# Optimization experiments

Measured on AMD Instinct MI355X. Metric: run time of the kernel, lower is better.

The kernel has to match this reference:

```python
import jax, jax.numpy as jnp
from jax import lax
import numpy as np

NEG = -1e30  # safe log-space -inf for fp32 (avoids inf-inf NaNs)
EPS = 1e-7   # keras.backend.epsilon()


def setup_inputs() -> dict:
    key = jax.random.key(0)
    k1, k2 = jax.random.split(key)
    B, T, C, L = 512, 512, 96, 64
    y_true = jax.random.randint(k1, (B, L), 0, C - 1, dtype=jnp.int64)  # labels in [0, C-2]
    # y_pred mimics softmax output: positive, rows sum to 1
    logits = jax.random.uniform(k2, (B, T, C), dtype=jnp.float32)
    y_pred = logits / jnp.sum(logits, axis=-1, keepdims=True)
    return {"y_true": y_true, "y_pred": y_pred}


def _ctc_batch_cost(y_true, y_pred):
    # Faithful to keras.backend.ctc_batch_cost with full input/label lengths
    # and blank index = num_classes - 1.
    B, T, C = y_pred.shape
    L = y_true.shape[1]
    blank = C - 1
    S = 2 * L + 1  # extended label length: blanks interleaved

    logp = jnp.log(y_pred + EPS)  # [B, T, C]

    # extended label sequence: blank, l0, blank, l1, ..., blank
    ext = jnp.full((B, S), blank, dtype=y_true.dtype).at[:, 1::2].set(y_true)  # [B, S]

    # log-probs of extended labels at every time step: [T, B, S]
    lp = jnp.take_along_axis(
        logp, jnp.broadcast_to(ext[:, None, :], (B, T, S)), axis=2
    ).transpose(1, 0, 2)

    # skip transition (s-2 -> s) allowed iff ext[s] != blank and ext[s] != ext[s-2]
    skip = jnp.concatenate(
        [jnp.zeros((B, 2), dtype=bool),
         (ext[:, 2:] != blank) & (ext[:, 2:] != ext[:, :-2])],
        axis=1,
    )  # [B, S]

    # init: alpha_0(0) = logp(blank), alpha_0(1) = logp(l0)
    alpha0 = jnp.full((B, S), NEG, dtype=logp.dtype)
    alpha0 = alpha0.at[:, 0].set(lp[0, :, 0]).at[:, 1].set(lp[0, :, 1])

    def step(alpha, lp_t):
        s1 = jnp.pad(alpha[:, :-1], ((0, 0), (1, 0)), constant_values=NEG)
        s2 = jnp.pad(alpha[:, :-2], ((0, 0), (2, 0)), constant_values=NEG)
        a = jnp.logaddexp(alpha, s1)
        a = jnp.where(skip, jnp.logaddexp(a, s2), a)
        return a + lp_t, None

    alpha, _ = lax.scan(step, alpha0, lp[1:])
    loss = -jnp.logaddexp(alpha[:, -1], alpha[:, -2])  # [B]
    return loss[:, None]  # [B, 1], matching ctc_batch_cost


def reference(y_true, y_pred):
    return _ctc_batch_cost(y_true, y_pred)
```

## Files before the change

### kernel.cpp

```cpp
#include <hip/hip_runtime.h>
#include <math.h>


constexpr int Bv = 512;
constexpr int Tv = 512;
constexpr int Cv = 96;
constexpr int Lv = 64;
constexpr int BLANK = Cv - 1;
constexpr float EPSf = 1e-7f;

constexpr int ROWS = 32;
constexpr int NCH  = Tv / ROWS;
constexpr int CF   = ROWS * Cv;

__device__ __forceinline__ float dpp_shr1(float x) {
    return __int_as_float(
        __builtin_amdgcn_update_dpp(0, __float_as_int(x), 0x138, 0xf, 0xf, true));
}
template <int C>
__device__ __forceinline__ float dppmax(float m) {
    return fmaxf(m, __int_as_float(
        __builtin_amdgcn_update_dpp(0, __float_as_int(m), C, 0xf, 0xf, true)));
}

__global__ void __launch_bounds__(64) ctc_fwd(const int* __restrict__ y_true,
                                              const float* __restrict__ y_pred,
                                              float* __restrict__ out) {
    __shared__ float sink_lds[CF];

    const int b = blockIdx.x;
    const int l = threadIdx.x;
    const float* __restrict__ yp = y_pred + (size_t)b * (Tv * Cv);

    const int lab   = y_true[b * Lv + l];
    const int labm1 = __shfl_up(lab, 1);
    const bool skip = (l > 0) && (lab != labm1);

    const float* __restrict__ gB = yp + BLANK;
    const float* __restrict__ gL = yp + lab;

    float4 G0,G1,G2,G3,G4,G5,G6,G7,G8,G9,G10,G11;
    float4 H0,H1,H2,H3,H4,H5,H6,H7,H8,H9,H10,H11;
#define GLOAD(S, g) do { const float* gp_ = (g) + l * 4;                     \
    S##0 = *(const float4*)(gp_ +    0); S##1 = *(const float4*)(gp_ +  256);\
    S##2 = *(const float4*)(gp_ +  512); S##3 = *(const float4*)(gp_ +  768);\
    S##4 = *(const float4*)(gp_ + 1024); S##5 = *(const float4*)(gp_ + 1280);\
    S##6 = *(const float4*)(gp_ + 1536); S##7 = *(const float4*)(gp_ + 1792);\
    S##8 = *(const float4*)(gp_ + 2048); S##9 = *(const float4*)(gp_ + 2304);\
    S##10= *(const float4*)(gp_ + 2560); S##11= *(const float4*)(gp_ + 2816);\
    } while (0)
#define SINK(S) do { float4* sp_ = (float4*)sink_lds + l;                    \
    sp_[0]   = S##0; sp_[64]  = S##1; sp_[128] = S##2; sp_[192] = S##3;      \
    sp_[256] = S##4; sp_[320] = S##5; sp_[384] = S##6; sp_[448] = S##7;      \
    sp_[512] = S##8; sp_[576] = S##9; sp_[640] = S##10; sp_[704] = S##11;    \
    } while (0)

    GLOAD(G, yp);
    GLOAD(H, yp + CF);

    float PB0,PB1,PB2,PB3,PB4,PB5,PB6,PB7, PL0,PL1,PL2,PL3,PL4,PL5,PL6,PL7;
    float QB0,QB1,QB2,QB3,QB4,QB5,QB6,QB7, QL0,QL1,QL2,QL3,QL4,QL5,QL6,QL7;
#define LOADG(P, g) do {                                                     \
    const float* pB_ = gB + (size_t)(8 * (g)) * Cv;                          \
    const float* pL_ = gL + (size_t)(8 * (g)) * Cv;                          \
    P##B0 = pB_[0*Cv]; P##L0 = pL_[0*Cv]; P##B1 = pB_[1*Cv]; P##L1 = pL_[1*Cv];\
    P##B2 = pB_[2*Cv]; P##L2 = pL_[2*Cv]; P##B3 = pB_[3*Cv]; P##L3 = pL_[3*Cv];\
    P##B4 = pB_[4*Cv]; P##L4 = pL_[4*Cv]; P##B5 = pB_[5*Cv]; P##L5 = pL_[5*Cv];\
    P##B6 = pB_[6*Cv]; P##L6 = pL_[6*Cv]; P##B7 = pB_[7*Cv]; P##L7 = pL_[7*Cv];\
    } while (0)

    LOADG(P, 0);
    LOADG(Q, 1);

    float a0, a1, a2;
    int   e_acc = 0;
    float sc_p = 1.0f; int e_p = 0;

    auto step = [&](float PB, float PL) {
        float pb  = PB + EPSf;
        float pl  = PL + EPSf;
        float a1p = dpp_shr1(a1);
        float na0 = (a0 + a1p) * pb;
        float s1  = a0 + a1 + (skip ? a1p : 0.0f);
        float na1 = s1 * pl;
        float na2 = (a2 + a1) * pb;
        a0 = na0; a1 = na1; a2 = na2;
    };
    auto rn_apply = [&]() {
        a0 *= sc_p; a1 *= sc_p; a2 *= sc_p; e_acc += e_p;
    };
    auto rn_compute = [&]() {
        float m = fmaxf(fmaxf(a0, a1), a2);
        m = dppmax<0x111>(m); m = dppmax<0x112>(m); m = dppmax<0x114>(m);
        m = dppmax<0x118>(m); m = dppmax<0x142>(m); m = dppmax<0x143>(m);
        float mw = __int_as_float(__builtin_amdgcn_readlane(__float_as_int(m), 63));
        unsigned ef = __float_as_uint(mw) >> 23;
        e_p  = (int)ef - 126;
        sc_p = __uint_as_float((253u - ef) << 23);
    };

#define STEP_PF(P, i) do { step(P##B##i, P##L##i);                           \
    P##B##i = pB2[(i) * Cv]; P##L##i = pL2[(i) * Cv]; } while (0)
#define GROUP(P, g) do {                                                     \
    int r20_ = 8 * ((g) + 2); if (r20_ > Tv - 8) r20_ = Tv - 8;              \
    const float* pB2 = gB + (size_t)r20_ * Cv;                               \
    const float* pL2 = gL + (size_t)r20_ * Cv;                               \
    STEP_PF(P,0); STEP_PF(P,1); STEP_PF(P,2); STEP_PF(P,3); rn_apply();      \
    STEP_PF(P,4); STEP_PF(P,5); STEP_PF(P,6); STEP_PF(P,7); rn_compute();    \
    } while (0)

    {
        const bool lane0 = (l == 0);
        a0 = lane0 ? (PB0 + EPSf) : 0.0f;
        a1 = lane0 ? (PL0 + EPSf) : 0.0f;
        a2 = 0.0f;
        const float* pB2 = gB + (size_t)16 * Cv;
        const float* pL2 = gL + (size_t)16 * Cv;
        PB0 = pB2[0]; PL0 = pL2[0];
        STEP_PF(P,1); STEP_PF(P,2); STEP_PF(P,3); rn_apply();
        STEP_PF(P,4); STEP_PF(P,5); STEP_PF(P,6); STEP_PF(P,7); rn_compute();
    }

    SINK(G); GLOAD(G, yp + 2 * CF);
    GROUP(Q, 1); GROUP(P, 2); GROUP(Q, 3);

    for (int c = 1; c < NCH; ++c) {
        if (c <= NCH - 3) {
            if (c & 1) { SINK(H); GLOAD(H, yp + (size_t)(c + 2) * CF); }
            else       { SINK(G); GLOAD(G, yp + (size_t)(c + 2) * CF); }
        }
        int g = 4 * c;
        GROUP(P, g); GROUP(Q, g + 1); GROUP(P, g + 2); GROUP(Q, g + 3);
    }

    if (l == 63) {
        float sum = a1 + a2;
        out[b] = -(logf(sum) + (float)e_acc * 0.69314718055994530942f);
    }
#undef GLOAD
#undef SINK
#undef LOADG
#undef STEP_PF
#undef GROUP
}

extern "C" void kernel_launch(void* const* d_in, const int* in_sizes, int n_in,
                              void* d_out, int out_size, void* d_ws, size_t ws_size,
                              hipStream_t stream) {
    const int*   y_true = (const int*)d_in[0];
    const float* y_pred = (const float*)d_in[1];
    float*       out    = (float*)d_out;
    (void)in_sizes; (void)n_in; (void)out_size; (void)d_ws; (void)ws_size;
    ctc_fwd<<<Bv, 64, 0, stream>>>(y_true, y_pred, out);
}
```

Measured before the change: 158.8 us.

## Split into producer waves streaming y_pred chunks into an LDS ring for a consumer wave

```diff
diff --git a/kernel.cpp b/kernel.cpp
--- a/kernel.cpp
+++ b/kernel.cpp
@@ -12,6 +12,9 @@
 constexpr int ROWS = 32;
 constexpr int NCH  = Tv / ROWS;
 constexpr int CF   = ROWS * Cv;
+constexpr int RS   = 100;
+constexpr int SLOTF = ROWS * RS;
+constexpr int NSLOT = 4;
 
 __device__ __forceinline__ float dpp_shr1(float x) {
     return __int_as_float(
@@ -23,54 +26,64 @@
         __builtin_amdgcn_update_dpp(0, __float_as_int(m), C, 0xf, 0xf, true)));
 }
 
-__global__ void __launch_bounds__(64) ctc_fwd(const int* __restrict__ y_true,
-                                              const float* __restrict__ y_pred,
-                                              float* __restrict__ out) {
-    __shared__ float sink_lds[CF];
+__global__ void __launch_bounds__(256, 2) ctc_fwd(const int* __restrict__ y_true,
+                                                  const float* __restrict__ y_pred,
+                                                  float* __restrict__ out) {
+    __shared__ float ring[NSLOT * SLOTF];
+    __shared__ int   flags[8];
 
     const int b = blockIdx.x;
-    const int l = threadIdx.x;
+    const int w = threadIdx.x >> 6;
+    const int l = threadIdx.x & 63;
     const float* __restrict__ yp = y_pred + (size_t)b * (Tv * Cv);
+
+    if (threadIdx.x < 8) flags[threadIdx.x] = 0;
+    __syncthreads();
+
+    if (w != 0) {
+#define WA(i) ((((i)*64 + l) / 24) * (RS * 4) + (((i)*64 + l) % 24) * 16)
+        const int wa0 = WA(0),  wa1 = WA(1),  wa2 = WA(2),  wa3 = WA(3);
+        const int wa4 = WA(4),  wa5 = WA(5),  wa6 = WA(6),  wa7 = WA(7);
+        const int wa8 = WA(8),  wa9 = WA(9), wa10 = WA(10), wa11 = WA(11);
+#undef WA
+        float4 G0,G1,G2,G3,G4,G5,G6,G7,G8,G9,G10,G11;
+#define GLOAD(g) do { const float* gp_ = (g) + l * 4;                        \
+    G0 = *(const float4*)(gp_ +    0); G1 = *(const float4*)(gp_ +  256);    \
+    G2 = *(const float4*)(gp_ +  512); G3 = *(const float4*)(gp_ +  768);    \
+    G4 = *(const float4*)(gp_ + 1024); G5 = *(const float4*)(gp_ + 1280);    \
+    G6 = *(const float4*)(gp_ + 1536); G7 = *(const float4*)(gp_ + 1792);    \
+    G8 = *(const float4*)(gp_ + 2048); G9 = *(const float4*)(gp_ + 2304);    \
+    G10= *(const float4*)(gp_ + 2560); G11= *(const float4*)(gp_ + 2816);    \
+    } while (0)
+#define SWRITE(base) do { char* p_ = (char*)(base);                          \
+    *(float4*)(p_ + wa0) = G0;  *(float4*)(p_ + wa1) = G1;                   \
+    *(float4*)(p_ + wa2) = G2;  *(float4*)(p_ + wa3) = G3;                   \
+    *(float4*)(p_ + wa4) = G4;  *(float4*)(p_ + wa5) = G5;                   \
+    *(float4*)(p_ + wa6) = G6;  *(float4*)(p_ + wa7) = G7;                   \
+    *(float4*)(p_ + wa8) = G8;  *(float4*)(p_ + wa9) = G9;                   \
+    *(float4*)(p_ + wa10)= G10; *(float4*)(p_ + wa11)= G11; } while (0)
+
+        volatile int* cd = &flags[4];
+        int c = w - 1;
+        GLOAD(yp + (size_t)c * CF);
+        while (c < NCH) {
+            while (*cd < c - (NSLOT - 1)) __builtin_amdgcn_s_sleep(8);
+            SWRITE((char*)ring + (size_t)(c & (NSLOT - 1)) * (SLOTF * 4));
+            __builtin_amdgcn_s_waitcnt(0xC07F);
+            __asm__ __volatile__("" ::: "memory");
+            if (l == 0) *((volatile int*)&flags[c & (NSLOT - 1)]) = c + 1;
+            c += 3;
+            if (c < NCH) GLOAD(yp + (size_t)c * CF);
+        }
+#undef GLOAD
+#undef SWRITE
+        return;
+    }
 
     const int lab   = y_true[b * Lv + l];
     const int labm1 = __shfl_up(lab, 1);
     const bool skip = (l > 0) && (lab != labm1);
-
-    const float* __restrict__ gB = yp + BLANK;
-    const float* __restrict__ gL = yp + lab;
-
-    float4 G0,G1,G2,G3,G4,G5,G6,G7,G8,G9,G10,G11;
-    float4 H0,H1,H2,H3,H4,H5,H6,H7,H8,H9,H10,H11;
-#define GLOAD(S, g) do { const float* gp_ = (g) + l * 4;                     \
-    S##0 = *(const float4*)(gp_ +    0); S##1 = *(const float4*)(gp_ +  256);\
-    S##2 = *(const float4*)(gp_ +  512); S##3 = *(const float4*)(gp_ +  768);\
-    S##4 = *(const float4*)(gp_ + 1024); S##5 = *(const float4*)(gp_ + 1280);\
-    S##6 = *(const float4*)(gp_ + 1536); S##7 = *(const float4*)(gp_ + 1792);\
-    S##8 = *(const float4*)(gp_ + 2048); S##9 = *(const float4*)(gp_ + 2304);\
-    S##10= *(const float4*)(gp_ + 2560); S##11= *(const float4*)(gp_ + 2816);\
-    } while (0)
-#define SINK(S) do { float4* sp_ = (float4*)sink_lds + l;                    \
-    sp_[0]   = S##0; sp_[64]  = S##1; sp_[128] = S##2; sp_[192] = S##3;      \
-    sp_[256] = S##4; sp_[320] = S##5; sp_[384] = S##6; sp_[448] = S##7;      \
-    sp_[512] = S##8; sp_[576] = S##9; sp_[640] = S##10; sp_[704] = S##11;    \
-    } while (0)
-
-    GLOAD(G, yp);
-    GLOAD(H, yp + CF);
-
-    float PB0,PB1,PB2,PB3,PB4,PB5,PB6,PB7, PL0,PL1,PL2,PL3,PL4,PL5,PL6,PL7;
-    float QB0,QB1,QB2,QB3,QB4,QB5,QB6,QB7, QL0,QL1,QL2,QL3,QL4,QL5,QL6,QL7;
-#define LOADG(P, g) do {                                                     \
-    const float* pB_ = gB + (size_t)(8 * (g)) * Cv;                          \
-    const float* pL_ = gL + (size_t)(8 * (g)) * Cv;                          \
-    P##B0 = pB_[0*Cv]; P##L0 = pL_[0*Cv]; P##B1 = pB_[1*Cv]; P##L1 = pL_[1*Cv];\
-    P##B2 = pB_[2*Cv]; P##L2 = pL_[2*Cv]; P##B3 = pB_[3*Cv]; P##L3 = pL_[3*Cv];\
-    P##B4 = pB_[4*Cv]; P##L4 = pL_[4*Cv]; P##B5 = pB_[5*Cv]; P##L5 = pL_[5*Cv];\
-    P##B6 = pB_[6*Cv]; P##L6 = pL_[6*Cv]; P##B7 = pB_[7*Cv]; P##L7 = pL_[7*Cv];\
-    } while (0)
-
-    LOADG(P, 0);
-    LOADG(Q, 1);
+    const bool lane0 = (l == 0);
 
     float a0, a1, a2;
     int   e_acc = 0;
@@ -86,9 +99,7 @@
         float na2 = (a2 + a1) * pb;
         a0 = na0; a1 = na1; a2 = na2;
     };
-    auto rn_apply = [&]() {
-        a0 *= sc_p; a1 *= sc_p; a2 *= sc_p; e_acc += e_p;
-    };
+    auto rn_apply = [&]() { a0 *= sc_p; a1 *= sc_p; a2 *= sc_p; e_acc += e_p; };
     auto rn_compute = [&]() {
         float m = fmaxf(fmaxf(a0, a1), a2);
         m = dppmax<0x111>(m); m = dppmax<0x112>(m); m = dppmax<0x114>(m);
@@ -99,49 +110,75 @@
         sc_p = __uint_as_float((253u - ef) << 23);
     };
 
-#define STEP_PF(P, i) do { step(P##B##i, P##L##i);                           \
-    P##B##i = pB2[(i) * Cv]; P##L##i = pL2[(i) * Cv]; } while (0)
-#define GROUP(P, g) do {                                                     \
-    int r20_ = 8 * ((g) + 2); if (r20_ > Tv - 8) r20_ = Tv - 8;              \
-    const float* pB2 = gB + (size_t)r20_ * Cv;                               \
-    const float* pL2 = gL + (size_t)r20_ * Cv;                               \
-    STEP_PF(P,0); STEP_PF(P,1); STEP_PF(P,2); STEP_PF(P,3); rn_apply();      \
-    STEP_PF(P,4); STEP_PF(P,5); STEP_PF(P,6); STEP_PF(P,7); rn_compute();    \
+    float PB0,PB1,PB2,PB3,PB4,PB5,PB6,PB7, PL0,PL1,PL2,PL3,PL4,PL5,PL6,PL7;
+    float QB0,QB1,QB2,QB3,QB4,QB5,QB6,QB7, QL0,QL1,QL2,QL3,QL4,QL5,QL6,QL7;
+#define LOAD8(P, sb, r0) do {                                                \
+    const float* pB_ = (sb) + (r0) * RS + BLANK;                             \
+    const float* pL_ = (sb) + (r0) * RS + lab;                               \
+    P##B0 = pB_[0*RS]; P##L0 = pL_[0*RS]; P##B1 = pB_[1*RS]; P##L1 = pL_[1*RS];\
+    P##B2 = pB_[2*RS]; P##L2 = pL_[2*RS]; P##B3 = pB_[3*RS]; P##L3 = pL_[3*RS];\
+    P##B4 = pB_[4*RS]; P##L4 = pL_[4*RS]; P##B5 = pB_[5*RS]; P##L5 = pL_[5*RS];\
+    P##B6 = pB_[6*RS]; P##L6 = pL_[6*RS]; P##B7 = pB_[7*RS]; P##L7 = pL_[7*RS];\
     } while (0)
+#define STEP_RL(P, i) do { step(P##B##i, P##L##i);                           \
+    P##B##i = rb_[(i) * RS]; P##L##i = rl_[(i) * RS]; } while (0)
+#define GROUP_RL(P, sb, r16) do {                                            \
+    const float* rb_ = (sb) + (r16) * RS + BLANK;                            \
+    const float* rl_ = (sb) + (r16) * RS + lab;                              \
+    STEP_RL(P,0); STEP_RL(P,1); STEP_RL(P,2); STEP_RL(P,3); rn_apply();      \
+    STEP_RL(P,4); STEP_RL(P,5); STEP_RL(P,6); STEP_RL(P,7); rn_compute();    \
+    } while (0)
+#define GROUP_N(P) do {                                                      \
+    step(P##B0,P##L0); step(P##B1,P##L1); step(P##B2,P##L2); step(P##B3,P##L3);\
+    rn_apply();                                                              \
+    step(P##B4,P##L4); step(P##B5,P##L5); step(P##B6,P##L6); step(P##B7,P##L7);\
+    rn_compute(); } while (0)
 
+    volatile int* vf = flags;
+
+    while (vf[0] != 1) __builtin_amdgcn_s_sleep(8);
+    __asm__ __volatile__("" ::: "memory");
     {
-        const bool lane0 = (l == 0);
+        const float* sb = ring;
+        LOAD8(P, sb, 0); LOAD8(Q, sb, 8);
         a0 = lane0 ? (PB0 + EPSf) : 0.0f;
         a1 = lane0 ? (PL0 + EPSf) : 0.0f;
         a2 = 0.0f;
-        const float* pB2 = gB + (size_t)16 * Cv;
-        const float* pL2 = gL + (size_t)16 * Cv;
-        PB0 = pB2[0]; PL0 = pL2[0];
-        STEP_PF(P,1); STEP_PF(P,2); STEP_PF(P,3); rn_apply();
-        STEP_PF(P,4); STEP_PF(P,5); STEP_PF(P,6); STEP_PF(P,7); rn_compute();
+        {
+            const float* rb_ = sb + 16 * RS + BLANK;
+            const float* rl_ = sb + 16 * RS + lab;
+            PB0 = rb_[0]; PL0 = rl_[0];
+            STEP_RL(P,1); STEP_RL(P,2); STEP_RL(P,3); rn_apply();
+            STEP_RL(P,4); STEP_RL(P,5); STEP_RL(P,6); STEP_RL(P,7); rn_compute();
+        }
+        GROUP_RL(Q, sb, 24);
+        GROUP_N(P);
+        GROUP_N(Q);
     }
-
-    SINK(G); GLOAD(G, yp + 2 * CF);
-    GROUP(Q, 1); GROUP(P, 2); GROUP(Q, 3);
+    __asm__ __volatile__("" ::: "memory");
+    if (l == 0) *((volatile int*)&flags[4]) = 1;
 
     for (int c = 1; c < NCH; ++c) {
-        if (c <= NCH - 3) {
-            if (c & 1) { SINK(H); GLOAD(H, yp + (size_t)(c + 2) * CF); }
-            else       { SINK(G); GLOAD(G, yp + (size_t)(c + 2) * CF); }
-        }
-        int g = 4 * c;
-        GROUP(P, g); GROUP(Q, g + 1); GROUP(P, g + 2); GROUP(Q, g + 3);
+        while (vf[c & (NSLOT - 1)] != c + 1) __builtin_amdgcn_s_sleep(8);
+        __asm__ __volatile__("" ::: "memory");
+        const float* sb = ring + (size_t)(c & (NSLOT - 1)) * SLOTF;
+        LOAD8(P, sb, 0); LOAD8(Q, sb, 8);
+        GROUP_RL(P, sb, 16);
+        GROUP_RL(Q, sb, 24);
+        GROUP_N(P);
+        GROUP_N(Q);
+        __asm__ __volatile__("" ::: "memory");
+        if (l == 0) *((volatile int*)&flags[4]) = c + 1;
     }
 
     if (l == 63) {
         float sum = a1 + a2;
         out[b] = -(logf(sum) + (float)e_acc * 0.69314718055994530942f);
     }
-#undef GLOAD
-#undef SINK
-#undef LOADG
-#undef STEP_PF
-#undef GROUP
+#undef LOAD8
+#undef STEP_RL
+#undef GROUP_RL
+#undef GROUP_N
 }
 
 extern "C" void kernel_launch(void* const* d_in, const int* in_sizes, int n_in,
@@ -151,5 +188,5 @@
     const float* y_pred = (const float*)d_in[1];
     float*       out    = (float*)d_out;
     (void)in_sizes; (void)n_in; (void)out_size; (void)d_ws; (void)ws_size;
-    ctc_fwd<<<Bv, 64, 0, stream>>>(y_true, y_pred, out);
+    ctc_fwd<<<Bv, 256, 0, stream>>>(y_true, y_pred, out);
 }
```

After: 153.9 us. 1.03x faster.
